# Kernel optimization log

Hardware: AMD Instinct MI355X
Metric: run time of the kernel (lower is better)

## Reference

```python
import jax, jax.numpy as jnp
import numpy as np

N, E, D_IN, D_HID, D_OUT = 50000, 800000, 128, 128, 300
BN_EPS = 1e-5


def setup_inputs() -> dict:
    key = jax.random.key(0)
    ks = jax.random.split(key, 10)
    s_in = 1.0 / np.sqrt(D_IN)
    s_hid = 1.0 / np.sqrt(D_HID)
    return {
        "x": jax.random.normal(ks[0], (N, D_IN), jnp.float32),
        "edge_index": jax.random.randint(ks[1], (2, E), 0, N, jnp.int64),
        "Wl": jax.random.normal(ks[2], (D_IN, D_HID), jnp.float32) * s_in,
        "bl": jnp.zeros((D_HID,), jnp.float32),
        "Wr": jax.random.normal(ks[3], (D_IN, D_HID), jnp.float32) * s_in,
        "Wsk": jax.random.normal(ks[4], (D_IN, D_HID), jnp.float32) * s_in,
        "bsk": jnp.zeros((D_HID,), jnp.float32),
        "gamma": jnp.ones((D_HID,), jnp.float32),
        "beta": jnp.zeros((D_HID,), jnp.float32),
        "rmean": jnp.zeros((D_HID,), jnp.float32),
        "rvar": jnp.ones((D_HID,), jnp.float32),
        "Wlo": jax.random.normal(ks[5], (D_HID, D_OUT), jnp.float32) * s_hid,
        "blo": jnp.zeros((D_OUT,), jnp.float32),
        "Wro": jax.random.normal(ks[6], (D_HID, D_OUT), jnp.float32) * s_hid,
    }


def sage_conv(x, src, dst, n_nodes, W_l, b_l, W_r):
    # PyG SAGEConv (aggr='mean'): lin_l(mean_{j in N(i)} x_j) + lin_r(x_i)
    msgs = x[src]                                                 # [E, d] gather
    agg = jax.ops.segment_sum(msgs, dst, num_segments=n_nodes)    # [N, d]
    cnt = jax.ops.segment_sum(jnp.ones((src.shape[0], 1), x.dtype), dst,
                              num_segments=n_nodes)               # [N, 1]
    mean = agg / jnp.maximum(cnt, 1.0)
    return mean @ W_l + b_l + x @ W_r


def reference(x, edge_index, Wl, bl, Wr, Wsk, bsk, gamma, beta, rmean, rvar,
              Wlo, blo, Wro):
    src, dst = edge_index[0], edge_index[1]
    n = x.shape[0]
    # layer 0: conv + skip linear
    h = sage_conv(x, src, dst, n, Wl, bl, Wr) + (x @ Wsk + bsk)
    # BatchNorm1d (eval: running stats)
    h = (h - rmean) * (gamma * jax.lax.rsqrt(rvar + BN_EPS)) + beta
    x_emb = jax.nn.relu(h)                                        # dropout: no-op in eval
    # output conv + log_softmax
    x_out = sage_conv(x_emb, src, dst, n, Wlo, blo, Wro)
    return h, jax.nn.log_softmax(x_out, axis=1)
```

## Files before the change

### kernel.cpp

```cpp
#include <hip/hip_runtime.h>

typedef __attribute__((__ext_vector_type__(8))) __bf16 bf16x8;
typedef __attribute__((__ext_vector_type__(4))) float f32x4;
typedef __attribute__((__ext_vector_type__(2))) float f32x2;
typedef __attribute__((__ext_vector_type__(4))) unsigned int u32x4;

__device__ __forceinline__ float bf2f(unsigned short u) {
    return __uint_as_float(((unsigned int)u) << 16);
}
__device__ __forceinline__ unsigned short f2bf(float f) {
    unsigned int u = __float_as_uint(f);
    u += 0x7FFFu + ((u >> 16) & 1u);
    return (unsigned short)(u >> 16);
}

__device__ __forceinline__ bool low_short_is_bf16like(unsigned int w) {
    unsigned int lo = w & 0xFFFFu;
    if (lo == 0u || lo == 0x8000u) return true;
    unsigned int e = (lo >> 7) & 0xFFu;
    return (e >= 0x6Cu && e <= 0x8Cu);
}
__device__ __forceinline__ int probe_f32(const unsigned int* __restrict__ p) {
    int t = threadIdx.x & 63;
    int cnt = __popcll(__ballot(low_short_is_bf16like(p[t])));
    return (cnt < 32) ? 1 : 0;
}
__device__ __forceinline__ int probe_e64(const unsigned int* __restrict__ ei) {
    int t = threadIdx.x & 63;
    unsigned int o1 = ei[2 * t + 1];
    unsigned int o2 = ei[2 * t + 129];
    return __all((o1 == 0u) && (o2 == 0u)) ? 1 : 0;
}

__device__ __forceinline__ void front_rank(
    int blk, int t, const int* __restrict__ ei, int* __restrict__ deg,
    int* __restrict__ rank, unsigned int* __restrict__ ds32,
    int E, int nnodes, int pack)
{
    int e64 = probe_e64((const unsigned int*)ei);
    int e = blk * 256 + t;
    if (e >= E) return;
    int s, d;
    if (e64) { s = ei[2 * e]; d = ei[2 * (E + e)]; }
    else     { s = ei[e];     d = ei[E + e]; }
    if ((unsigned)s >= (unsigned)nnodes) s = 0;
    int r = 0;
    if ((unsigned)d < (unsigned)nnodes) r = atomicAdd(&deg[d], 1);
    rank[e] = r;
    if (pack) ds32[e] = (((unsigned int)d & 0xFFFFu) << 16) | ((unsigned int)s & 0xFFFFu);
}

__device__ __forceinline__ void front_tobf(
    int blk, int t, const void* __restrict__ xv,
    unsigned short* __restrict__ xbf, unsigned int* __restrict__ x8, long nelem)
{
    int xf32 = probe_f32((const unsigned int*)xv);
    long i = ((long)blk * 256 + t) * 8;
    if (i >= nelem) return;
    float f[8];
    if (xf32) {
        const float4* p = (const float4*)((const float*)xv + i);
        float4 v0 = p[0], v1 = p[1];
        f[0] = v0.x; f[1] = v0.y; f[2] = v0.z; f[3] = v0.w;
        f[4] = v1.x; f[5] = v1.y; f[6] = v1.z; f[7] = v1.w;
        u32x4 o;
        o.x = (unsigned int)f2bf(f[0]) | ((unsigned int)f2bf(f[1]) << 16);
        o.y = (unsigned int)f2bf(f[2]) | ((unsigned int)f2bf(f[3]) << 16);
        o.z = (unsigned int)f2bf(f[4]) | ((unsigned int)f2bf(f[5]) << 16);
        o.w = (unsigned int)f2bf(f[6]) | ((unsigned int)f2bf(f[7]) << 16);
        *(u32x4*)&xbf[i] = o;
    } else {
        u32x4 v = *(const u32x4*)((const unsigned short*)xv + i);
        *(u32x4*)&xbf[i] = v;
        f[0] = bf2f((unsigned short)v.x); f[1] = bf2f((unsigned short)(v.x >> 16));
        f[2] = bf2f((unsigned short)v.y); f[3] = bf2f((unsigned short)(v.y >> 16));
        f[4] = bf2f((unsigned short)v.z); f[5] = bf2f((unsigned short)(v.z >> 16));
        f[6] = bf2f((unsigned short)v.w); f[7] = bf2f((unsigned short)(v.w >> 16));
    }
    unsigned int q0 = 0, q1 = 0;
    q0 = (unsigned int)__builtin_amdgcn_cvt_pk_fp8_f32(f[0], f[1], (int)q0, false);
    q0 = (unsigned int)__builtin_amdgcn_cvt_pk_fp8_f32(f[2], f[3], (int)q0, true);
    q1 = (unsigned int)__builtin_amdgcn_cvt_pk_fp8_f32(f[4], f[5], (int)q1, false);
    q1 = (unsigned int)__builtin_amdgcn_cvt_pk_fp8_f32(f[6], f[7], (int)q1, true);
    uint2 q; q.x = q0; q.y = q1;
    *(uint2*)&x8[i >> 2] = q;
}

__global__ __launch_bounds__(256) void k_front(
    const int* __restrict__ ei, int* __restrict__ deg, int* __restrict__ rank,
    unsigned int* __restrict__ ds32, int E, int nnodes, int pack, int egrid,
    const void* __restrict__ xv, unsigned short* __restrict__ xbf,
    unsigned int* __restrict__ x8, long nelem, int tgrid,
    const void* __restrict__ Wl, const void* __restrict__ Wr,
    const void* __restrict__ Wsk, const void* __restrict__ gamma,
    const void* __restrict__ rvar, const void* __restrict__ bl,
    const void* __restrict__ bsk, const void* __restrict__ rmean,
    const void* __restrict__ beta, const void* __restrict__ Wlo,
    const void* __restrict__ blo, const void* __restrict__ Wro,
    unsigned short* __restrict__ W1p, unsigned short* __restrict__ W2p,
    float* __restrict__ bias1, float* __restrict__ bias2)
{
    int blk = blockIdx.x, t = threadIdx.x;
    int mn = (egrid < tgrid) ? egrid : tgrid;
    int m2 = 2 * mn;
    if (blk < m2) {
        if (blk & 1) front_tobf(blk >> 1, t, xv, xbf, x8, nelem);
        else         front_rank(blk >> 1, t, ei, deg, rank, ds32, E, nnodes, pack);
        return;
    }
    if (blk < egrid + tgrid) {
        int r = blk - m2;
        if (egrid > tgrid) front_rank(mn + r, t, ei, deg, rank, ds32, E, nnodes, pack);
        else               front_tobf(mn + r, t, xv, xbf, x8, nelem);
        return;
    }
    int wf32 = probe_f32((const unsigned int*)Wl);
    int b = blk - egrid - tgrid;
    if (b < 128) {
        int idx = b * 256 + t;
        int kb = idx >> 10, c = (idx >> 3) & 127, k7 = idx & 7;
        int k = kb * 8 + k7;
        float g, rv, w;
        if (wf32) {
            g  = ((const float*)gamma)[c];
            rv = ((const float*)rvar)[c];
            if (k < 128) w = ((const float*)Wl)[k * 128 + c];
            else { int kk = k - 128;
                   w = ((const float*)Wr)[kk * 128 + c] + ((const float*)Wsk)[kk * 128 + c]; }
        } else {
            g  = bf2f(((const unsigned short*)gamma)[c]);
            rv = bf2f(((const unsigned short*)rvar)[c]);
            if (k < 128) w = bf2f(((const unsigned short*)Wl)[k * 128 + c]);
            else { int kk = k - 128;
                   w = bf2f(((const unsigned short*)Wr)[kk * 128 + c]) +
                       bf2f(((const unsigned short*)Wsk)[kk * 128 + c]); }
        }
        float s = g * rsqrtf(rv + 1e-5f);
        W1p[idx] = f2bf(w * s);
    } else if (b < 448) {
        int idx = (b - 128) * 256 + t;
        int kb = idx / 2560;
        int rem = idx - kb * 2560;
        int c = rem >> 3, k7 = idx & 7;
        int k = kb * 8 + k7;
        float w = 0.f;
        if (c < 300) {
            if (wf32)
                w = (k < 128) ? ((const float*)Wlo)[k * 300 + c]
                              : ((const float*)Wro)[(k - 128) * 300 + c];
            else
                w = (k < 128) ? bf2f(((const unsigned short*)Wlo)[k * 300 + c])
                              : bf2f(((const unsigned short*)Wro)[(k - 128) * 300 + c]);
        }
        W2p[idx] = f2bf(w);
    } else {
        if (t < 128) {
            float g, rv, b1, b2, rm, be;
            if (wf32) {
                g = ((const float*)gamma)[t]; rv = ((const float*)rvar)[t];
                b1 = ((const float*)bl)[t];   b2 = ((const float*)bsk)[t];
                rm = ((const float*)rmean)[t]; be = ((const float*)beta)[t];
            } else {
                g = bf2f(((const unsigned short*)gamma)[t]); rv = bf2f(((const unsigned short*)rvar)[t]);
                b1 = bf2f(((const unsigned short*)bl)[t]);   b2 = bf2f(((const unsigned short*)bsk)[t]);
                rm = bf2f(((const unsigned short*)rmean)[t]); be = bf2f(((const unsigned short*)beta)[t]);
            }
            float s = g * rsqrtf(rv + 1e-5f);
            bias1[t] = (b1 + b2 - rm) * s + be;
        }
        for (int c = t; c < 320; c += 256) {
            float v = 0.f;
            if (c < 300)
                v = wf32 ? ((const float*)blo)[c] : bf2f(((const unsigned short*)blo)[c]);
            bias2[c] = v;
        }
    }
}

__global__ __launch_bounds__(256) void k_scan(
    const int* __restrict__ deg, int* __restrict__ rowptr,
    int* __restrict__ aux, int* __restrict__ scnt, int n, int nblk)
{
    __shared__ int wsum[4];
    __shared__ int lastflag;
    int t = threadIdx.x, blk = blockIdx.x;
    int base = blk * 1024 + t * 4;
    int v[4];
    int s = 0;
    #pragma unroll
    for (int i = 0; i < 4; i++) { int idx = base + i; v[i] = (idx < n) ? deg[idx] : 0; s += v[i]; }
    int lane = t & 63, wv = t >> 6;
    int inc = s;
    #pragma unroll
    for (int off = 1; off < 64; off <<= 1) {
        int u = __shfl_up(inc, off);
        if (lane >= off) inc += u;
    }
    if (lane == 63) wsum[wv] = inc;
    __syncthreads();
    int woff = 0;
    if (wv >= 1) woff += wsum[0];
    if (wv >= 2) woff += wsum[1];
    if (wv >= 3) woff += wsum[2];
    int exc = woff + inc - s;
    #pragma unroll
    for (int i = 0; i < 4; i++) { int idx = base + i; if (idx < n) rowptr[idx] = exc; exc += v[i]; }
    if (t == 255) {
        aux[blk] = woff + inc;
        __threadfence();
        int prev = atomicAdd(scnt, 1);
        lastflag = (prev == nblk - 1) ? 1 : 0;
    }
    __syncthreads();
    if (lastflag && t < 64) {
        __threadfence();
        int carry = 0;
        for (int b2 = 0; b2 < nblk; b2 += 64) {
            int idx = b2 + t;
            int av = (idx < nblk) ? aux[idx] : 0;
            int inc2 = av;
            #pragma unroll
            for (int off = 1; off < 64; off <<= 1) {
                int u = __shfl_up(inc2, off);
                if (t >= off) inc2 += u;
            }
            if (idx < nblk) aux[idx] = carry + inc2 - av;
            carry += __shfl(inc2, 63);
        }
    }
}

__global__ __launch_bounds__(256) void k_place16(
    const unsigned int* __restrict__ ds32,
    const int* __restrict__ rowptr, const int* __restrict__ aux,
    const int* __restrict__ rank,
    unsigned short* __restrict__ adj, int E, int nnodes)
{
    int e = blockIdx.x * 256 + threadIdx.x;
    if (e >= E) return;
    unsigned int ds = ds32[e];
    int d = (int)(ds >> 16);
    unsigned short s = (unsigned short)(ds & 0xFFFFu);
    if (d >= nnodes) return;
    adj[rowptr[d] + aux[d >> 10] + rank[e]] = s;
}

__global__ __launch_bounds__(256) void k_place32(
    const int* __restrict__ ei,
    const int* __restrict__ rowptr, const int* __restrict__ aux,
    const int* __restrict__ rank,
    int* __restrict__ adj, int E, int nnodes)
{
    int e64 = probe_e64((const unsigned int*)ei);
    int e = blockIdx.x * 256 + threadIdx.x;
    if (e >= E) return;
    int s, d;
    if (e64) { s = ei[2 * e]; d = ei[2 * (E + e)]; }
    else     { s = ei[e];     d = ei[E + e]; }
    if ((unsigned)d >= (unsigned)nnodes) return;
    if ((unsigned)s >= (unsigned)nnodes) s = 0;
    adj[rowptr[d] + aux[d >> 10] + rank[e]] = s;
}

template <typename IT>
__global__ __launch_bounds__(256) void k_agg(
    const unsigned int* __restrict__ x8,
    const int* __restrict__ rowptr, const int* __restrict__ aux,
    const int* __restrict__ deg,
    const IT* __restrict__ adj, unsigned short* __restrict__ meanB, int n)
{
    int wid = (blockIdx.x * 256 + threadIdx.x) >> 6;
    if (wid >= n) return;
    int lane = threadIdx.x & 63;
    int h  = lane >> 5;
    int sl = lane & 31;
    int start = rowptr[wid] + aux[wid >> 10];
    int dc = deg[wid];
    float acc[4][4];
    #pragma unroll
    for (int u = 0; u < 4; u++)
        #pragma unroll
        for (int c = 0; c < 4; c++) acc[u][c] = 0.f;
    int i = 0;
    for (; i + 15 < dc; i += 16) {
        int e[8]; unsigned int p[8];
        #pragma unroll
        for (int u = 0; u < 8; u++) e[u] = (int)adj[start + i + 2 * u + h];
        #pragma unroll
        for (int u = 0; u < 8; u++) p[u] = x8[(size_t)e[u] * 32 + sl];
        #pragma unroll
        for (int u = 0; u < 8; u++) {
            f32x2 lo = __builtin_amdgcn_cvt_pk_f32_fp8((int)p[u], false);
            f32x2 hi = __builtin_amdgcn_cvt_pk_f32_fp8((int)p[u], true);
            acc[u & 3][0] += lo.x; acc[u & 3][1] += lo.y;
            acc[u & 3][2] += hi.x; acc[u & 3][3] += hi.y;
        }
    }
    if (i + 7 < dc) {
        int e[4]; unsigned int p[4];
        #pragma unroll
        for (int u = 0; u < 4; u++) e[u] = (int)adj[start + i + 2 * u + h];
        #pragma unroll
        for (int u = 0; u < 4; u++) p[u] = x8[(size_t)e[u] * 32 + sl];
        #pragma unroll
        for (int u = 0; u < 4; u++) {
            f32x2 lo = __builtin_amdgcn_cvt_pk_f32_fp8((int)p[u], false);
            f32x2 hi = __builtin_amdgcn_cvt_pk_f32_fp8((int)p[u], true);
            acc[u][0] += lo.x; acc[u][1] += lo.y;
            acc[u][2] += hi.x; acc[u][3] += hi.y;
        }
        i += 8;
    }
    for (; i + h < dc; i += 2) {
        int e0 = (int)adj[start + i + h];
        unsigned int p0 = x8[(size_t)e0 * 32 + sl];
        f32x2 lo = __builtin_amdgcn_cvt_pk_f32_fp8((int)p0, false);
        f32x2 hi = __builtin_amdgcn_cvt_pk_f32_fp8((int)p0, true);
        acc[0][0] += lo.x; acc[0][1] += lo.y; acc[0][2] += hi.x; acc[0][3] += hi.y;
    }
    float t0 = (acc[0][0] + acc[1][0]) + (acc[2][0] + acc[3][0]);
    float t1 = (acc[0][1] + acc[1][1]) + (acc[2][1] + acc[3][1]);
    float t2 = (acc[0][2] + acc[1][2]) + (acc[2][2] + acc[3][2]);
    float t3 = (acc[0][3] + acc[1][3]) + (acc[2][3] + acc[3][3]);
    t0 += __shfl_xor(t0, 32);
    t1 += __shfl_xor(t1, 32);
    t2 += __shfl_xor(t2, 32);
    t3 += __shfl_xor(t3, 32);
    if (h == 0) {
        float inv = 1.f / fmaxf((float)dc, 1.f);
        uint2 o;
        o.x = (unsigned int)f2bf(t0 * inv) | ((unsigned int)f2bf(t1 * inv) << 16);
        o.y = (unsigned int)f2bf(t2 * inv) | ((unsigned int)f2bf(t3 * inv) << 16);
        *(uint2*)&meanB[(size_t)wid * 128 + sl * 4] = o;
    }
}

__global__ __launch_bounds__(256) void k_gemm1(
    const unsigned short* __restrict__ meanB,
    const unsigned short* __restrict__ xbf, const unsigned int* __restrict__ xprobe,
    const unsigned short* __restrict__ Wp,
    const float* __restrict__ bias, void* __restrict__ outh,
    unsigned int* __restrict__ xemb8, int nrows)
{
    constexpr int NTW = 2;
    __shared__ __align__(16) unsigned short Alds[32 * 264];
    int tid = threadIdx.x;
    int row0 = blockIdx.x * 32;
    int xf32 = probe_f32(xprobe);
    {
        int r = tid >> 3, c0 = (tid & 7) * 16;
        int rg = row0 + r; if (rg >= nrows) rg = nrows - 1;
        const u32x4* mp = (const u32x4*)(meanB + (size_t)rg * 128 + c0);
        *(u32x4*)&Alds[r * 264 + c0]     = mp[0];
        *(u32x4*)&Alds[r * 264 + c0 + 8] = mp[1];
        const u32x4* xp = (const u32x4*)(xbf + (size_t)rg * 128 + c0);
        *(u32x4*)&Alds[r * 264 + 128 + c0]     = xp[0];
        *(u32x4*)&Alds[r * 264 + 128 + c0 + 8] = xp[1];
    }
    __syncthreads();
    f32x4 acc[2][NTW];
    #pragma unroll
    for (int a = 0; a < 2; a++)
        #pragma unroll
        for (int b = 0; b < NTW; b++) acc[a][b] = f32x4{0.f, 0.f, 0.f, 0.f};
    int lane = tid & 63, wv = tid >> 6, lh = lane & 15, lq = lane >> 4;
    bf16x8 bcur[NTW], bnxt[NTW];
    #pragma unroll
    for (int i = 0; i < NTW; i++)
        bcur[i] = *(const bf16x8*)&Wp[lq * 1024 + ((wv + 4 * i) * 16 + lh) * 8];
    #pragma unroll
    for (int ks = 0; ks < 8; ++ks) {
        if (ks < 7) {
            #pragma unroll
            for (int i = 0; i < NTW; i++)
                bnxt[i] = *(const bf16x8*)&Wp[((ks + 1) * 4 + lq) * 1024 + ((wv + 4 * i) * 16 + lh) * 8];
        }
        bf16x8 a0 = *(const bf16x8*)&Alds[lh * 264 + ks * 32 + lq * 8];
        bf16x8 a1 = *(const bf16x8*)&Alds[(16 + lh) * 264 + ks * 32 + lq * 8];
        #pragma unroll
        for (int i = 0; i < NTW; i++) {
            acc[0][i] = __builtin_amdgcn_mfma_f32_16x16x32_bf16(a0, bcur[i], acc[0][i], 0, 0, 0);
            acc[1][i] = __builtin_amdgcn_mfma_f32_16x16x32_bf16(a1, bcur[i], acc[1][i], 0, 0, 0);
        }
        #pragma unroll
        for (int i = 0; i < NTW; i++) bcur[i] = bnxt[i];
    }
    __syncthreads();
    float* outF = (float*)outh;
    unsigned short* outB = (unsigned short*)outh;
    #pragma unroll
    for (int rt = 0; rt < 2; ++rt)
        #pragma unroll
        for (int i = 0; i < NTW; i++)
            #pragma unroll
            for (int j = 0; j < 4; j++) {
                int rl = rt * 16 + lq * 4 + j;
                int r = row0 + rl;
                int c = (wv + 4 * i) * 16 + lh;
                float v = acc[rt][i][j] + bias[c];
                Alds[rl * 264 + c] = f2bf(fmaxf(v, 0.f));
                if (r < nrows) {
                    if (xf32) __builtin_nontemporal_store(v, &outF[(size_t)r * 128 + c]);
                    else      outB[(size_t)r * 128 + c] = f2bf(v);
                }
            }
    __syncthreads();
    {
        int r = tid >> 3, c0 = (tid & 7) * 16;
        int rg = row0 + r;
        if (rg < nrows) {
            u32x4 va = *(u32x4*)&Alds[r * 264 + c0];
            u32x4 vb = *(u32x4*)&Alds[r * 264 + c0 + 8];
            u32x4 q;
            unsigned int w;
            w = 0;
            w = (unsigned int)__builtin_amdgcn_cvt_pk_fp8_f32(
                    bf2f((unsigned short)va.x), bf2f((unsigned short)(va.x >> 16)), (int)w, false);
            w = (unsigned int)__builtin_amdgcn_cvt_pk_fp8_f32(
                    bf2f((unsigned short)va.y), bf2f((unsigned short)(va.y >> 16)), (int)w, true);
            q.x = w;
            w = 0;
            w = (unsigned int)__builtin_amdgcn_cvt_pk_fp8_f32(
                    bf2f((unsigned short)va.z), bf2f((unsigned short)(va.z >> 16)), (int)w, false);
            w = (unsigned int)__builtin_amdgcn_cvt_pk_fp8_f32(
                    bf2f((unsigned short)va.w), bf2f((unsigned short)(va.w >> 16)), (int)w, true);
            q.y = w;
            w = 0;
            w = (unsigned int)__builtin_amdgcn_cvt_pk_fp8_f32(
                    bf2f((unsigned short)vb.x), bf2f((unsigned short)(vb.x >> 16)), (int)w, false);
            w = (unsigned int)__builtin_amdgcn_cvt_pk_fp8_f32(
                    bf2f((unsigned short)vb.y), bf2f((unsigned short)(vb.y >> 16)), (int)w, true);
            q.z = w;
            w = 0;
            w = (unsigned int)__builtin_amdgcn_cvt_pk_fp8_f32(
                    bf2f((unsigned short)vb.z), bf2f((unsigned short)(vb.z >> 16)), (int)w, false);
            w = (unsigned int)__builtin_amdgcn_cvt_pk_fp8_f32(
                    bf2f((unsigned short)vb.w), bf2f((unsigned short)(vb.w >> 16)), (int)w, true);
            q.w = w;
            *(u32x4*)&xemb8[(size_t)rg * 32 + (tid & 7) * 4] = q;
        }
    }
}

__global__ __launch_bounds__(256) void k_gemm2(
    const unsigned short* __restrict__ meanB,
    const unsigned int* __restrict__ xemb8, const unsigned int* __restrict__ xprobe,
    const unsigned short* __restrict__ Wp,
    const float* __restrict__ bias, void* __restrict__ outbase, int nrows)
{
    constexpr int NTW = 5;
    __shared__ __align__(16) unsigned short Alds[16 * 264];
    __shared__ float redM[4][16];
    __shared__ float redS[4][16];
    int tid = threadIdx.x;
    int row0 = blockIdx.x * 16;
    int xf32 = probe_f32(xprobe);
    {
        int r = tid >> 4, c0 = (tid & 15) * 8;
        int rg = row0 + r; if (rg >= nrows) rg = nrows - 1;
        *(u32x4*)&Alds[r * 264 + c0] = *(const u32x4*)(meanB + (size_t)rg * 128 + c0);
        uint2 q = *(const uint2*)&xemb8[(size_t)rg * 32 + (c0 >> 2)];
        #pragma unroll
        for (int k = 0; k < 2; k++) {
            unsigned int w = (k == 0) ? q.x : q.y;
            f32x2 lo = __builtin_amdgcn_cvt_pk_f32_fp8((int)w, false);
            f32x2 hi = __builtin_amdgcn_cvt_pk_f32_fp8((int)w, true);
            unsigned int p0 = (unsigned int)f2bf(lo.x) | ((unsigned int)f2bf(lo.y) << 16);
            unsigned int p1 = (unsigned int)f2bf(hi.x) | ((unsigned int)f2bf(hi.y) << 16);
            *(unsigned int*)&Alds[r * 264 + 128 + c0 + k * 4]     = p0;
            *(unsigned int*)&Alds[r * 264 + 128 + c0 + k * 4 + 2] = p1;
        }
    }
    __syncthreads();
    f32x4 acc[NTW];
    #pragma unroll
    for (int b = 0; b < NTW; b++) acc[b] = f32x4{0.f, 0.f, 0.f, 0.f};
    int lane = tid & 63, wv = tid >> 6, lh = lane & 15, lq = lane >> 4;
    bf16x8 bcur[NTW], bnxt[NTW];
    #pragma unroll
    for (int i = 0; i < NTW; i++)
        bcur[i] = *(const bf16x8*)&Wp[lq * 2560 + ((wv + 4 * i) * 16 + lh) * 8];
    #pragma unroll
    for (int ks = 0; ks < 8; ++ks) {
        if (ks < 7) {
            #pragma unroll
            for (int i = 0; i < NTW; i++)
                bnxt[i] = *(const bf16x8*)&Wp[((ks + 1) * 4 + lq) * 2560 + ((wv + 4 * i) * 16 + lh) * 8];
        }
        bf16x8 a0 = *(const bf16x8*)&Alds[lh * 264 + ks * 32 + lq * 8];
        #pragma unroll
        for (int i = 0; i < NTW; i++)
            acc[i] = __builtin_amdgcn_mfma_f32_16x16x32_bf16(a0, bcur[i], acc[i], 0, 0, 0);
        #pragma unroll
        for (int i = 0; i < NTW; i++) bcur[i] = bnxt[i];
    }
    #pragma unroll
    for (int i = 0; i < NTW; i++) {
        int col = (wv + 4 * i) * 16 + lh;
        float b = bias[col];
        #pragma unroll
        for (int j = 0; j < 4; j++) acc[i][j] += b;
    }
    float M[4];
    #pragma unroll
    for (int j = 0; j < 4; j++) {
        float m = -3.0e38f;
        #pragma unroll
        for (int i = 0; i < NTW; i++) {
            int col = (wv + 4 * i) * 16 + lh;
            if (col < 300) m = fmaxf(m, acc[i][j]);
        }
        m = fmaxf(m, __shfl_xor(m, 1, 16));
        m = fmaxf(m, __shfl_xor(m, 2, 16));
        m = fmaxf(m, __shfl_xor(m, 4, 16));
        m = fmaxf(m, __shfl_xor(m, 8, 16));
        M[j] = m;
    }
    if (lh == 0) {
        #pragma unroll
        for (int j = 0; j < 4; j++) redM[wv][lq * 4 + j] = M[j];
    }
    __syncthreads();
    #pragma unroll
    for (int j = 0; j < 4; j++) {
        int rl = lq * 4 + j;
        M[j] = fmaxf(fmaxf(redM[0][rl], redM[1][rl]),
                     fmaxf(redM[2][rl], redM[3][rl]));
    }
    float S[4];
    #pragma unroll
    for (int j = 0; j < 4; j++) {
        float s = 0.f;
        #pragma unroll
        for (int i = 0; i < NTW; i++) {
            int col = (wv + 4 * i) * 16 + lh;
            if (col < 300) s += __expf(acc[i][j] - M[j]);
        }
        s += __shfl_xor(s, 1, 16);
        s += __shfl_xor(s, 2, 16);
        s += __shfl_xor(s, 4, 16);
        s += __shfl_xor(s, 8, 16);
        S[j] = s;
    }
    if (lh == 0) {
        #pragma unroll
        for (int j = 0; j < 4; j++) redS[wv][lq * 4 + j] = S[j];
    }
    __syncthreads();
    float* out1F = (float*)outbase + (size_t)nrows * 128;
    unsigned short* out1B = (unsigned short*)outbase + (size_t)nrows * 128;
    #pragma unroll
    for (int j = 0; j < 4; j++) {
        int rl = lq * 4 + j;
        float Sall = (redS[0][rl] + redS[1][rl]) + (redS[2][rl] + redS[3][rl]);
        float L = M[j] + __logf(Sall);
        int rg = row0 + rl;
        if (rg < nrows) {
            #pragma unroll
            for (int i = 0; i < NTW; i++) {
                int col = (wv + 4 * i) * 16 + lh;
                if (col < 300) {
                    float v = acc[i][j] - L;
                    if (xf32) out1F[(size_t)rg * 300 + col] = v;
                    else      out1B[(size_t)rg * 300 + col] = f2bf(v);
                }
            }
        }
    }
}

extern "C" void kernel_launch(void* const* d_in, const int* in_sizes, int n_in,
                              void* d_out, int out_size, void* d_ws, size_t ws_size,
                              hipStream_t stream)
{
    const void* x     = d_in[0];
    const int*  ei    = (const int*)d_in[1];
    const void* Wl    = d_in[2];
    const void* bl    = d_in[3];
    const void* Wr    = d_in[4];
    const void* Wsk   = d_in[5];
    const void* bsk   = d_in[6];
    const void* gamma = d_in[7];
    const void* beta  = d_in[8];
    const void* rmean = d_in[9];
    const void* rvar  = d_in[10];
    const void* Wlo   = d_in[11];
    const void* blo   = d_in[12];
    const void* Wro   = d_in[13];

    int N = in_sizes[0] / 128;
    int E = in_sizes[1] / 2;
    long nelem = (long)N * 128;
    bool idx16 = (N <= 65535);

    char* ws = (char*)d_ws;
    size_t off = 0;
    unsigned short* xbf   = (unsigned short*)(ws + off); off += (size_t)N * 128 * 2;
    unsigned short* meanB = (unsigned short*)(ws + off); off += (size_t)N * 128 * 2;
    unsigned int* x8      = (unsigned int*)(ws + off);   off += (size_t)N * 128;
    unsigned int* xemb8   = (unsigned int*)(ws + off);   off += (size_t)N * 128;
    off = (off + 255) & ~(size_t)255;
    int* deg    = (int*)(ws + off);           off += (size_t)N * 4;
    int* scnt   = (int*)(ws + off);           off += 256;
    int* rowptr = (int*)(ws + off);           off += (size_t)N * 4;
    int* rank   = (int*)(ws + off);           off += (size_t)E * 4;
    unsigned int* ds32 = (unsigned int*)(ws + off); off += (size_t)E * 4;
    int* aux    = (int*)(ws + off);           off += 256;
    void* adjv  = (void*)(ws + off);          off += (size_t)E * 4;
    off = (off + 255) & ~(size_t)255;
    unsigned short* W1p = (unsigned short*)(ws + off);  off += 32768 * 2;
    unsigned short* W2p = (unsigned short*)(ws + off);  off += 81920 * 2;
    float* bias1 = (float*)(ws + off);        off += 512;
    float* bias2 = (float*)(ws + off);        off += 1280;

    int egrid  = (E + 255) / 256;
    int sblk   = (N + 1023) / 1024;
    int agrid  = (N + 3) / 4;
    int g1grid = (N + 31) / 32;
    int g2grid = (N + 15) / 16;
    int tgrid  = (int)((nelem / 8 + 255) / 256);

    const unsigned int* xprobe = (const unsigned int*)x;

    hipMemsetAsync(deg, 0, (size_t)N * 4 + 256, stream);

    k_front<<<egrid + tgrid + 449, 256, 0, stream>>>(
        ei, deg, rank, ds32, E, N, idx16 ? 1 : 0, egrid,
        x, xbf, x8, nelem, tgrid,
        Wl, Wr, Wsk, gamma, rvar, bl, bsk, rmean, beta, Wlo, blo, Wro,
        W1p, W2p, bias1, bias2);

    k_scan<<<sblk, 256, 0, stream>>>(deg, rowptr, aux, scnt, N, sblk);

    if (idx16) {
        unsigned short* adj = (unsigned short*)adjv;
        k_place16<<<egrid, 256, 0, stream>>>(ds32, rowptr, aux, rank, adj, E, N);
        k_agg<unsigned short><<<agrid, 256, 0, stream>>>(x8, rowptr, aux, deg, adj, meanB, N);
        k_gemm1<<<g1grid, 256, 0, stream>>>(meanB, xbf, xprobe, W1p, bias1, d_out, xemb8, N);
        k_agg<unsigned short><<<agrid, 256, 0, stream>>>(xemb8, rowptr, aux, deg, adj, meanB, N);
        k_gemm2<<<g2grid, 256, 0, stream>>>(meanB, xemb8, xprobe, W2p, bias2, d_out, N);
    } else {
        int* adj = (int*)adjv;
        k_place32<<<egrid, 256, 0, stream>>>(ei, rowptr, aux, rank, adj, E, N);
        k_agg<int><<<agrid, 256, 0, stream>>>(x8, rowptr, aux, deg, adj, meanB, N);
        k_gemm1<<<g1grid, 256, 0, stream>>>(meanB, xbf, xprobe, W1p, bias1, d_out, xemb8, N);
        k_agg<int><<<agrid, 256, 0, stream>>>(xemb8, rowptr, aux, deg, adj, meanB, N);
        k_gemm2<<<g2grid, 256, 0, stream>>>(meanB, xemb8, xprobe, W2p, bias2, d_out, N);
    }
}
```

Measured before the change: 159.6 us.

## Fuse neighbor mean aggregation into both GEMM kernels via LDS

```diff
diff --git a/kernel.cpp b/kernel.cpp
--- a/kernel.cpp
+++ b/kernel.cpp
@@ -30,6 +30,74 @@
     unsigned int o1 = ei[2 * t + 1];
     unsigned int o2 = ei[2 * t + 129];
     return __all((o1 == 0u) && (o2 == 0u)) ? 1 : 0;
+}
+
+template <typename IT>
+__device__ __forceinline__ void gather_mean_to_lds(
+    const unsigned int* __restrict__ x8,
+    const int* __restrict__ rowptr, const int* __restrict__ aux,
+    const int* __restrict__ deg, const IT* __restrict__ adj,
+    int rg, int h, int sl, unsigned short* __restrict__ ldsrow)
+{
+    int start = rowptr[rg] + aux[rg >> 10];
+    int dc = deg[rg];
+    float acc[4][4];
+    #pragma unroll
+    for (int u = 0; u < 4; u++)
+        #pragma unroll
+        for (int c = 0; c < 4; c++) acc[u][c] = 0.f;
+    int i = 0;
+    for (; i + 15 < dc; i += 16) {
+        int e[8]; unsigned int p[8];
+        #pragma unroll
+        for (int u = 0; u < 8; u++) e[u] = (int)adj[start + i + 2 * u + h];
+        #pragma unroll
+        for (int u = 0; u < 8; u++) p[u] = x8[(size_t)e[u] * 32 + sl];
+        #pragma unroll
+        for (int u = 0; u < 8; u++) {
+            f32x2 lo = __builtin_amdgcn_cvt_pk_f32_fp8((int)p[u], false);
+            f32x2 hi = __builtin_amdgcn_cvt_pk_f32_fp8((int)p[u], true);
+            acc[u & 3][0] += lo.x; acc[u & 3][1] += lo.y;
+            acc[u & 3][2] += hi.x; acc[u & 3][3] += hi.y;
+        }
+    }
+    if (i + 7 < dc) {
+        int e[4]; unsigned int p[4];
+        #pragma unroll
+        for (int u = 0; u < 4; u++) e[u] = (int)adj[start + i + 2 * u + h];
+        #pragma unroll
+        for (int u = 0; u < 4; u++) p[u] = x8[(size_t)e[u] * 32 + sl];
+        #pragma unroll
+        for (int u = 0; u < 4; u++) {
+            f32x2 lo = __builtin_amdgcn_cvt_pk_f32_fp8((int)p[u], false);
+            f32x2 hi = __builtin_amdgcn_cvt_pk_f32_fp8((int)p[u], true);
+            acc[u][0] += lo.x; acc[u][1] += lo.y;
+            acc[u][2] += hi.x; acc[u][3] += hi.y;
+        }
+        i += 8;
+    }
+    for (; i + h < dc; i += 2) {
+        int e0 = (int)adj[start + i + h];
+        unsigned int p0 = x8[(size_t)e0 * 32 + sl];
+        f32x2 lo = __builtin_amdgcn_cvt_pk_f32_fp8((int)p0, false);
+        f32x2 hi = __builtin_amdgcn_cvt_pk_f32_fp8((int)p0, true);
+        acc[0][0] += lo.x; acc[0][1] += lo.y; acc[0][2] += hi.x; acc[0][3] += hi.y;
+    }
+    float t0 = (acc[0][0] + acc[1][0]) + (acc[2][0] + acc[3][0]);
+    float t1 = (acc[0][1] + acc[1][1]) + (acc[2][1] + acc[3][1]);
+    float t2 = (acc[0][2] + acc[1][2]) + (acc[2][2] + acc[3][2]);
+    float t3 = (acc[0][3] + acc[1][3]) + (acc[2][3] + acc[3][3]);
+    t0 += __shfl_xor(t0, 32);
+    t1 += __shfl_xor(t1, 32);
+    t2 += __shfl_xor(t2, 32);
+    t3 += __shfl_xor(t3, 32);
+    if (h == 0) {
+        float inv = 1.f / fmaxf((float)dc, 1.f);
+        uint2 o;
+        o.x = (unsigned int)f2bf(t0 * inv) | ((unsigned int)f2bf(t1 * inv) << 16);
+        o.y = (unsigned int)f2bf(t2 * inv) | ((unsigned int)f2bf(t3 * inv) << 16);
+        *(uint2*)&ldsrow[sl * 4] = o;
+    }
 }
 
 __device__ __forceinline__ void front_rank(
@@ -263,80 +331,10 @@
 }
 
 template <typename IT>
-__global__ __launch_bounds__(256) void k_agg(
+__global__ __launch_bounds__(256) void k_ag1(
     const unsigned int* __restrict__ x8,
     const int* __restrict__ rowptr, const int* __restrict__ aux,
-    const int* __restrict__ deg,
-    const IT* __restrict__ adj, unsigned short* __restrict__ meanB, int n)
-{
-    int wid = (blockIdx.x * 256 + threadIdx.x) >> 6;
-    if (wid >= n) return;
-    int lane = threadIdx.x & 63;
-    int h  = lane >> 5;
-    int sl = lane & 31;
-    int start = rowptr[wid] + aux[wid >> 10];
-    int dc = deg[wid];
-    float acc[4][4];
-    #pragma unroll
-    for (int u = 0; u < 4; u++)
-        #pragma unroll
-        for (int c = 0; c < 4; c++) acc[u][c] = 0.f;
-    int i = 0;
-    for (; i + 15 < dc; i += 16) {
-        int e[8]; unsigned int p[8];
-        #pragma unroll
-        for (int u = 0; u < 8; u++) e[u] = (int)adj[start + i + 2 * u + h];
-        #pragma unroll
-        for (int u = 0; u < 8; u++) p[u] = x8[(size_t)e[u] * 32 + sl];
-        #pragma unroll
-        for (int u = 0; u < 8; u++) {
-            f32x2 lo = __builtin_amdgcn_cvt_pk_f32_fp8((int)p[u], false);
-            f32x2 hi = __builtin_amdgcn_cvt_pk_f32_fp8((int)p[u], true);
-            acc[u & 3][0] += lo.x; acc[u & 3][1] += lo.y;
-            acc[u & 3][2] += hi.x; acc[u & 3][3] += hi.y;
-        }
-    }
-    if (i + 7 < dc) {
-        int e[4]; unsigned int p[4];
-        #pragma unroll
-        for (int u = 0; u < 4; u++) e[u] = (int)adj[start + i + 2 * u + h];
-        #pragma unroll
-        for (int u = 0; u < 4; u++) p[u] = x8[(size_t)e[u] * 32 + sl];
-        #pragma unroll
-        for (int u = 0; u < 4; u++) {
-            f32x2 lo = __builtin_amdgcn_cvt_pk_f32_fp8((int)p[u], false);
-            f32x2 hi = __builtin_amdgcn_cvt_pk_f32_fp8((int)p[u], true);
-            acc[u][0] += lo.x; acc[u][1] += lo.y;
-            acc[u][2] += hi.x; acc[u][3] += hi.y;
-        }
-        i += 8;
-    }
-    for (; i + h < dc; i += 2) {
-        int e0 = (int)adj[start + i + h];
-        unsigned int p0 = x8[(size_t)e0 * 32 + sl];
-        f32x2 lo = __builtin_amdgcn_cvt_pk_f32_fp8((int)p0, false);
-        f32x2 hi = __builtin_amdgcn_cvt_pk_f32_fp8((int)p0, true);
-        acc[0][0] += lo.x; acc[0][1] += lo.y; acc[0][2] += hi.x; acc[0][3] += hi.y;
-    }
-    float t0 = (acc[0][0] + acc[1][0]) + (acc[2][0] + acc[3][0]);
-    float t1 = (acc[0][1] + acc[1][1]) + (acc[2][1] + acc[3][1]);
-    float t2 = (acc[0][2] + acc[1][2]) + (acc[2][2] + acc[3][2]);
-    float t3 = (acc[0][3] + acc[1][3]) + (acc[2][3] + acc[3][3]);
-    t0 += __shfl_xor(t0, 32);
-    t1 += __shfl_xor(t1, 32);
-    t2 += __shfl_xor(t2, 32);
-    t3 += __shfl_xor(t3, 32);
-    if (h == 0) {
-        float inv = 1.f / fmaxf((float)dc, 1.f);
-        uint2 o;
-        o.x = (unsigned int)f2bf(t0 * inv) | ((unsigned int)f2bf(t1 * inv) << 16);
-        o.y = (unsigned int)f2bf(t2 * inv) | ((unsigned int)f2bf(t3 * inv) << 16);
-        *(uint2*)&meanB[(size_t)wid * 128 + sl * 4] = o;
-    }
-}
-
-__global__ __launch_bounds__(256) void k_gemm1(
-    const unsigned short* __restrict__ meanB,
+    const int* __restrict__ deg, const IT* __restrict__ adj,
     const unsigned short* __restrict__ xbf, const unsigned int* __restrict__ xprobe,
     const unsigned short* __restrict__ Wp,
     const float* __restrict__ bias, void* __restrict__ outh,
@@ -350,20 +348,26 @@
     {
         int r = tid >> 3, c0 = (tid & 7) * 16;
         int rg = row0 + r; if (rg >= nrows) rg = nrows - 1;
-        const u32x4* mp = (const u32x4*)(meanB + (size_t)rg * 128 + c0);
-        *(u32x4*)&Alds[r * 264 + c0]     = mp[0];
-        *(u32x4*)&Alds[r * 264 + c0 + 8] = mp[1];
         const u32x4* xp = (const u32x4*)(xbf + (size_t)rg * 128 + c0);
         *(u32x4*)&Alds[r * 264 + 128 + c0]     = xp[0];
         *(u32x4*)&Alds[r * 264 + 128 + c0 + 8] = xp[1];
     }
+    int lane = tid & 63, wv = tid >> 6, lh = lane & 15, lq = lane >> 4;
+    {
+        int h = lane >> 5, sl = lane & 31;
+        for (int k = 0; k < 8; k++) {
+            int rl = wv * 8 + k;
+            int rg = row0 + rl; if (rg >= nrows) rg = nrows - 1;
+            gather_mean_to_lds<IT>(x8, rowptr, aux, deg, adj, rg, h, sl,
+                                   &Alds[rl * 264]);
+        }
+    }
     __syncthreads();
     f32x4 acc[2][NTW];
     #pragma unroll
     for (int a = 0; a < 2; a++)
         #pragma unroll
         for (int b = 0; b < NTW; b++) acc[a][b] = f32x4{0.f, 0.f, 0.f, 0.f};
-    int lane = tid & 63, wv = tid >> 6, lh = lane & 15, lq = lane >> 4;
     bf16x8 bcur[NTW], bnxt[NTW];
     #pragma unroll
     for (int i = 0; i < NTW; i++)
@@ -442,9 +446,12 @@
     }
 }
 
-__global__ __launch_bounds__(256) void k_gemm2(
-    const unsigned short* __restrict__ meanB,
-    const unsigned int* __restrict__ xemb8, const unsigned int* __restrict__ xprobe,
+template <typename IT>
+__global__ __launch_bounds__(256) void k_ag2(
+    const unsigned int* __restrict__ xemb8,
+    const int* __restrict__ rowptr, const int* __restrict__ aux,
+    const int* __restrict__ deg, const IT* __restrict__ adj,
+    const unsigned int* __restrict__ xprobe,
     const unsigned short* __restrict__ Wp,
     const float* __restrict__ bias, void* __restrict__ outbase, int nrows)
 {
@@ -458,7 +465,6 @@
     {
         int r = tid >> 4, c0 = (tid & 15) * 8;
         int rg = row0 + r; if (rg >= nrows) rg = nrows - 1;
-        *(u32x4*)&Alds[r * 264 + c0] = *(const u32x4*)(meanB + (size_t)rg * 128 + c0);
         uint2 q = *(const uint2*)&xemb8[(size_t)rg * 32 + (c0 >> 2)];
         #pragma unroll
         for (int k = 0; k < 2; k++) {
@@ -471,11 +477,20 @@
             *(unsigned int*)&Alds[r * 264 + 128 + c0 + k * 4 + 2] = p1;
         }
     }
+    int lane = tid & 63, wv = tid >> 6, lh = lane & 15, lq = lane >> 4;
+    {
+        int h = lane >> 5, sl = lane & 31;
+        for (int k = 0; k < 4; k++) {
+            int rl = wv * 4 + k;
+            int rg = row0 + rl; if (rg >= nrows) rg = nrows - 1;
+            gather_mean_to_lds<IT>(xemb8, rowptr, aux, deg, adj, rg, h, sl,
+                                   &Alds[rl * 264]);
+        }
+    }
     __syncthreads();
     f32x4 acc[NTW];
     #pragma unroll
     for (int b = 0; b < NTW; b++) acc[b] = f32x4{0.f, 0.f, 0.f, 0.f};
-    int lane = tid & 63, wv = tid >> 6, lh = lane & 15, lq = lane >> 4;
     bf16x8 bcur[NTW], bnxt[NTW];
     #pragma unroll
     for (int i = 0; i < NTW; i++)
@@ -596,7 +611,6 @@
     char* ws = (char*)d_ws;
     size_t off = 0;
     unsigned short* xbf   = (unsigned short*)(ws + off); off += (size_t)N * 128 * 2;
-    unsigned short* meanB = (unsigned short*)(ws + off); off += (size_t)N * 128 * 2;
     unsigned int* x8      = (unsigned int*)(ws + off);   off += (size_t)N * 128;
     unsigned int* xemb8   = (unsigned int*)(ws + off);   off += (size_t)N * 128;
     off = (off + 255) & ~(size_t)255;
@@ -615,7 +629,6 @@
 
     int egrid  = (E + 255) / 256;
     int sblk   = (N + 1023) / 1024;
-    int agrid  = (N + 3) / 4;
     int g1grid = (N + 31) / 32;
     int g2grid = (N + 15) / 16;
     int tgrid  = (int)((nelem / 8 + 255) / 256);
@@ -635,16 +648,16 @@
     if (idx16) {
         unsigned short* adj = (unsigned short*)adjv;
         k_place16<<<egrid, 256, 0, stream>>>(ds32, rowptr, aux, rank, adj, E, N);
-        k_agg<unsigned short><<<agrid, 256, 0, stream>>>(x8, rowptr, aux, deg, adj, meanB, N);
-        k_gemm1<<<g1grid, 256, 0, stream>>>(meanB, xbf, xprobe, W1p, bias1, d_out, xemb8, N);
-        k_agg<unsigned short><<<agrid, 256, 0, stream>>>(xemb8, rowptr, aux, deg, adj, meanB, N);
-        k_gemm2<<<g2grid, 256, 0, stream>>>(meanB, xemb8, xprobe, W2p, bias2, d_out, N);
+        k_ag1<unsigned short><<<g1grid, 256, 0, stream>>>(
+            x8, rowptr, aux, deg, adj, xbf, xprobe, W1p, bias1, d_out, xemb8, N);
+        k_ag2<unsigned short><<<g2grid, 256, 0, stream>>>(
+            xemb8, rowptr, aux, deg, adj, xprobe, W2p, bias2, d_out, N);
     } else {
         int* adj = (int*)adjv;
         k_place32<<<egrid, 256, 0, stream>>>(ei, rowptr, aux, rank, adj, E, N);
-        k_agg<int><<<agrid, 256, 0, stream>>>(x8, rowptr, aux, deg, adj, meanB, N);
-        k_gemm1<<<g1grid, 256, 0, stream>>>(meanB, xbf, xprobe, W1p, bias1, d_out, xemb8, N);
-        k_agg<int><<<agrid, 256, 0, stream>>>(xemb8, rowptr, aux, deg, adj, meanB, N);
-        k_gemm2<<<g2grid, 256, 0, stream>>>(meanB, xemb8, xprobe, W2p, bias2, d_out, N);
-    }
-}
+        k_ag1<int><<<g1grid, 256, 0, stream>>>(
+            x8, rowptr, aux, deg, adj, xbf, xprobe, W1p, bias1, d_out, xemb8, N);
+        k_ag2<int><<<g2grid, 256, 0, stream>>>(
+            xemb8, rowptr, aux, deg, adj, xprobe, W2p, bias2, d_out, N);
+    }
+}
```

New measurement: 172.0 us. 1.08x slower.
